# Performance work log

Measured on AMD Instinct MI355X. Metric: run time of the kernel, lower is better.

Reference implementation:

```python
import jax, jax.numpy as jnp
import numpy as np

NGRAM = 16
SUB = 512  # bytes per sub-block


def byte2image(block, ngram=NGRAM):
    """block: (B, L) int -> (B, 1, ngram*8, L-ngram) float32 in [-1, 1]."""
    B, L = block.shape
    blk = block.astype(jnp.int32)
    # nxt[:, i] = blk[:, i+1], last column zero
    nxt = jnp.concatenate([blk[:, 1:], jnp.zeros((B, 1), jnp.int32)], axis=1)
    # 8 bit-shifted views of the byte stream
    shifts = jnp.stack(
        [((blk << s) & 255) + ((nxt >> (8 - s)) & 255) for s in range(8)],
        axis=1,
    )  # (B, 8, L)
    flat = shifts.reshape(B, -1)  # (B, 8*L)
    parts = [flat] + [jnp.roll(flat, -i, axis=1) for i in range(1, ngram)]
    stacked = jnp.concatenate(parts, axis=1).reshape(B, ngram * 8, L)
    result = stacked[:, :, :-ngram].astype(jnp.float32)
    result = (result / 255.0 - 0.5) / 0.5
    return result[:, None]  # (B, 1, ngram*8, L-ngram)


def byte2image_4k(block, ngram=NGRAM):
    """block: (B, 4096) -> (B, 8, ngram*8, 512-ngram)."""
    return jnp.concatenate(
        [byte2image(block[:, i * SUB:(i + 1) * SUB], ngram) for i in range(8)],
        axis=1,
    )


def setup_inputs() -> dict:
    key = jax.random.key(0)
    kx, kw = jax.random.split(key)
    x = jax.random.randint(kx, (256, 4096), 0, 256, dtype=jnp.int64)
    W = jax.random.normal(kw, (496, 64), dtype=jnp.float32) * 0.02
    return {"x": x, "W": W}


def reference(x, W):
    # ByteFormerWrapper.forward with block_size=4096: byte2image_4k then the
    # (opaque) model; model stood in by a linear head over the image width.
    img = byte2image_4k(x)                      # (B, 8, 128, 496)
    out = jnp.einsum('bchw,wo->bcho', img, W)   # (B, 8, 128, 64)
    return out
```

## Files before the change

kernel.cpp:

```cpp
#include <hip/hip_runtime.h>

typedef unsigned short u16;
typedef unsigned int u32;
typedef _Float16 half8 __attribute__((ext_vector_type(8)));
typedef __attribute__((ext_vector_type(4))) float floatx4;

#define LSTRIDE 72
#define BIMG (128 * LSTRIDE)

__global__ __launch_bounds__(256, 2) void byteformer_fused(
    const int* __restrict__ x, const float* __restrict__ Wm,
    float* __restrict__ out) {
  __shared__ __align__(16) u16 arena[4 * BIMG];
  __shared__ float part[256];
  __shared__ float csumsh[64];

  const int t = threadIdx.x;
  const int mtile = blockIdx.x;
  const int y = blockIdx.y;

  const int wave = t >> 6, lane = t & 63;
  const int wm = wave >> 1, wn = wave & 1;
  const int quad = lane >> 4, l16 = lane & 15;

  const int sA_sub = t >> 4;
  const int sA_kg  = (t >> 1) & 7;
  const int sA_qh  = t & 1;
  const long xrow = ((long)mtile * 16 + sA_sub) * 512;

  floatx4 acc[4][4];
  #pragma unroll
  for (int mt = 0; mt < 4; ++mt)
    #pragma unroll
    for (int nt = 0; nt < 4; ++nt)
      acc[mt][nt] = floatx4{0.f, 0.f, 0.f, 0.f};

  float csum_local = 0.0f;

  int4 ca, cb; int cc;
  float f[17];

  auto xload = [&](int kc) {
    const int base = kc * 64 + sA_kg * 8;
    ca = *(const int4*)&x[xrow + base];
    cb = *(const int4*)&x[xrow + base + 4];
    cc = (base + 8 < 512) ? x[xrow + base + 8] : 0;
  };

  auto wload = [&](int kc) {
    const int cbase = kc * 64 + 16 * wave - 2 * y - 1;
    #pragma unroll
    for (int j = 0; j < 17; ++j) {
      const int c = cbase + j;
      f[j] = (c >= 0 && c < 496) ? Wm[c * 64 + lane] : 0.0f;
    }
  };

  auto astage = [&](u16* dstb) {
    const u32 c0 = (u32)ca.x, c1 = (u32)ca.y, c2 = (u32)ca.z, c3 = (u32)ca.w;
    const u32 c4 = (u32)cb.x, c5 = (u32)cb.y, c6 = (u32)cb.z, c7 = (u32)cb.w;
    const u32 c8 = (u32)cc;
    const u32 P0 = ((c0 << 8) | c1) | (((c1 << 8) | c2) << 16);
    const u32 P1 = ((c2 << 8) | c3) | (((c3 << 8) | c4) << 16);
    const u32 P2 = ((c4 << 8) | c5) | (((c5 << 8) | c6) << 16);
    const u32 P3 = ((c6 << 8) | c7) | (((c7 << 8) | c8) << 16);
    u16* arow = &dstb[(sA_sub * 8 + sA_qh * 4) * LSTRIDE + sA_kg * 8];
    #pragma unroll
    for (int qi = 0; qi < 4; ++qi) {
      const int sh = 8 - (sA_qh * 4 + qi);
      int4 d;
      d.x = (int)(((P0 >> sh) & 0x00FF00FFu) | 0x64006400u);
      d.y = (int)(((P1 >> sh) & 0x00FF00FFu) | 0x64006400u);
      d.z = (int)(((P2 >> sh) & 0x00FF00FFu) | 0x64006400u);
      d.w = (int)(((P3 >> sh) & 0x00FF00FFu) | 0x64006400u);
      *(int4*)(arow + qi * LSTRIDE) = d;
    }
  };

  auto bstage = [&](u16* dstb) {
    u16 h[17];
    #pragma unroll
    for (int j = 0; j < 17; ++j)
      h[j] = __builtin_bit_cast(unsigned short, (_Float16)f[j]);
    #pragma unroll
    for (int j = 1; j <= 16; ++j) csum_local += f[j];
    #pragma unroll
    for (int g = 0; g < 2; ++g) {
      const int mgrp = 2 * wave + g;
      #pragma unroll
      for (int pp = 0; pp < 2; ++pp) {
        const int jb = g * 8 + 1 - pp;
        int4 d;
        d.x = (int)((u32)h[jb + 0] | ((u32)h[jb + 1] << 16));
        d.y = (int)((u32)h[jb + 2] | ((u32)h[jb + 3] << 16));
        d.z = (int)((u32)h[jb + 4] | ((u32)h[jb + 5] << 16));
        d.w = (int)((u32)h[jb + 6] | ((u32)h[jb + 7] << 16));
        *(int4*)&dstb[(pp * 64 + lane) * LSTRIDE + mgrp * 8] = d;
      }
    }
  };

  auto compute = [&](const u16* Ab, const u16* Bb) {
    #pragma unroll
    for (int ks = 0; ks < 2; ++ks) {
      const int koff = ks * 32 + quad * 8;
      half8 af[4], bf[4];
      #pragma unroll
      for (int mt = 0; mt < 4; ++mt)
        af[mt] = *(const half8*)&Ab[(wm * 64 + mt * 16 + l16) * LSTRIDE + koff];
      #pragma unroll
      for (int nt = 0; nt < 4; ++nt)
        bf[nt] = *(const half8*)&Bb[(wn * 64 + nt * 16 + l16) * LSTRIDE + koff];
      #pragma unroll
      for (int mt = 0; mt < 4; ++mt)
        #pragma unroll
        for (int nt = 0; nt < 4; ++nt)
          acc[mt][nt] = __builtin_amdgcn_mfma_f32_16x16x32_f16(
              af[mt], bf[nt], acc[mt][nt], 0, 0, 0);
    }
  };

  xload(0); wload(0);
  astage(arena); bstage(arena + 2 * BIMG);
  __syncthreads();

  #pragma unroll
  for (int kc = 0; kc < 8; ++kc) {
    u16* Acur = arena + (kc & 1) * BIMG;
    u16* Bcur = arena + (2 + (kc & 1)) * BIMG;
    u16* Anxt = arena + ((kc + 1) & 1) * BIMG;
    u16* Bnxt = arena + (2 + ((kc + 1) & 1)) * BIMG;
    if (kc < 7) { xload(kc + 1); wload(kc + 1); }
    compute(Acur, Bcur);
    if (kc < 7) { astage(Anxt); bstage(Bnxt); }
    __syncthreads();
  }

  const float S = 2.0f / 255.0f;
  const float K1 = 1024.0f * S + 1.0f;
  part[t] = csum_local;
  __syncthreads();
  if (t < 64)
    csumsh[t] = K1 * (part[t] + part[t + 64] + part[t + 128] + part[t + 192]);
  __syncthreads();

  float cs[4];
  #pragma unroll
  for (int nt = 0; nt < 4; ++nt) cs[nt] = csumsh[nt * 16 + l16];

  float* ep = (float*)arena;
  #pragma unroll
  for (int mt = 0; mt < 4; ++mt) {
    #pragma unroll
    for (int i = 0; i < 4; ++i) {
      const int mr = wm * 64 + mt * 16 + quad * 4 + i;
      const int sub_l = mr >> 3, q = mr & 7;
      const int rowbase = sub_l * 1040 + wn * 512 + q * 64 + l16;
      #pragma unroll
      for (int nt = 0; nt < 4; ++nt)
        ep[rowbase + nt * 16] = S * acc[mt][nt][i] - cs[nt];
    }
  }
  __syncthreads();

  const long outbase = (long)mtile * 16 * 8192 + (long)y * 1024;
  #pragma unroll
  for (int k2 = 0; k2 < 16; ++k2) {
    const float4 v =
        *(const float4*)((const char*)ep + k2 * 4160 + wave * 1024 + lane * 16);
    *(float4*)&out[outbase + (long)k2 * 8192 + wave * 256 + lane * 4] = v;
  }
}

extern "C" void kernel_launch(void* const* d_in, const int* in_sizes, int n_in,
                              void* d_out, int out_size, void* d_ws, size_t ws_size,
                              hipStream_t stream) {
  const int* x = (const int*)d_in[0];
  const float* Wm = (const float*)d_in[1];
  float* out = (float*)d_out;
  byteformer_fused<<<dim3(128, 8), dim3(256), 0, stream>>>(x, Wm, out);
}
```

Measured before the change: 108.7 us.

## Single-buffer LDS tiles, split W loads across k-steps, raise occupancy to 4 blocks

Shared memory drops from a double-buffered A/B arena to one A and one B tile, and launch bounds rise from 2 to 4 blocks per CU to get more waves resident. W loads are split into two halves whose latency is hidden behind the two MFMA k-steps, and the fp16 packing is done early into packed registers. The epilogue runs in two halves so it fits in the smaller arena. The cost is an extra barrier per k-chunk with no LDS double buffering, and tighter register limits that could cause spills.

```diff
diff --git a/kernel.cpp b/kernel.cpp
--- a/kernel.cpp
+++ b/kernel.cpp
@@ -6,14 +6,16 @@
 typedef __attribute__((ext_vector_type(4))) float floatx4;
 
 #define LSTRIDE 72
-#define BIMG (128 * LSTRIDE)
-
-__global__ __launch_bounds__(256, 2) void byteformer_fused(
+#define TILE (128 * LSTRIDE)
+
+__global__ __launch_bounds__(256, 4) void byteformer_fused(
     const int* __restrict__ x, const float* __restrict__ Wm,
     float* __restrict__ out) {
-  __shared__ __align__(16) u16 arena[4 * BIMG];
+  __shared__ __align__(16) u16 arena[2 * TILE];
   __shared__ float part[256];
   __shared__ float csumsh[64];
+  u16* As = arena;
+  u16* Bs = arena + TILE;
 
   const int t = threadIdx.x;
   const int mtile = blockIdx.x;
@@ -38,7 +40,8 @@
   float csum_local = 0.0f;
 
   int4 ca, cb; int cc;
-  float f[17];
+  float fv[17];
+  u32 hp[9];
 
   auto xload = [&](int kc) {
     const int base = kc * 64 + sA_kg * 8;
@@ -47,16 +50,45 @@
     cc = (base + 8 < 512) ? x[xrow + base + 8] : 0;
   };
 
-  auto wload = [&](int kc) {
+  auto wissueA = [&](int kc) {
     const int cbase = kc * 64 + 16 * wave - 2 * y - 1;
     #pragma unroll
-    for (int j = 0; j < 17; ++j) {
+    for (int j = 0; j < 9; ++j) {
       const int c = cbase + j;
-      f[j] = (c >= 0 && c < 496) ? Wm[c * 64 + lane] : 0.0f;
-    }
-  };
-
-  auto astage = [&](u16* dstb) {
+      fv[j] = (c >= 0 && c < 496) ? Wm[c * 64 + lane] : 0.0f;
+    }
+  };
+  auto wissueB = [&](int kc) {
+    const int cbase = kc * 64 + 16 * wave - 2 * y - 1;
+    #pragma unroll
+    for (int j = 9; j < 17; ++j) {
+      const int c = cbase + j;
+      fv[j] = (c >= 0 && c < 496) ? Wm[c * 64 + lane] : 0.0f;
+    }
+  };
+  auto wfinishA = [&]() {
+    #pragma unroll
+    for (int j = 1; j <= 8; ++j) csum_local += fv[j];
+    #pragma unroll
+    for (int i = 0; i < 4; ++i) {
+      u32 h0 = __builtin_bit_cast(unsigned short, (_Float16)fv[2 * i]);
+      u32 h1 = __builtin_bit_cast(unsigned short, (_Float16)fv[2 * i + 1]);
+      hp[i] = h0 | (h1 << 16);
+    }
+  };
+  auto wfinishB = [&]() {
+    #pragma unroll
+    for (int j = 9; j <= 16; ++j) csum_local += fv[j];
+    #pragma unroll
+    for (int i = 4; i < 8; ++i) {
+      u32 h0 = __builtin_bit_cast(unsigned short, (_Float16)fv[2 * i]);
+      u32 h1 = __builtin_bit_cast(unsigned short, (_Float16)fv[2 * i + 1]);
+      hp[i] = h0 | (h1 << 16);
+    }
+    hp[8] = (u32)__builtin_bit_cast(unsigned short, (_Float16)fv[16]);
+  };
+
+  auto astage = [&]() {
     const u32 c0 = (u32)ca.x, c1 = (u32)ca.y, c2 = (u32)ca.z, c3 = (u32)ca.w;
     const u32 c4 = (u32)cb.x, c5 = (u32)cb.y, c6 = (u32)cb.z, c7 = (u32)cb.w;
     const u32 c8 = (u32)cc;
@@ -64,7 +96,7 @@
     const u32 P1 = ((c2 << 8) | c3) | (((c3 << 8) | c4) << 16);
     const u32 P2 = ((c4 << 8) | c5) | (((c5 << 8) | c6) << 16);
     const u32 P3 = ((c6 << 8) | c7) | (((c7 << 8) | c8) << 16);
-    u16* arow = &dstb[(sA_sub * 8 + sA_qh * 4) * LSTRIDE + sA_kg * 8];
+    u16* arow = &As[(sA_sub * 8 + sA_qh * 4) * LSTRIDE + sA_kg * 8];
     #pragma unroll
     for (int qi = 0; qi < 4; ++qi) {
       const int sh = 8 - (sA_qh * 4 + qi);
@@ -77,63 +109,55 @@
     }
   };
 
-  auto bstage = [&](u16* dstb) {
-    u16 h[17];
-    #pragma unroll
-    for (int j = 0; j < 17; ++j)
-      h[j] = __builtin_bit_cast(unsigned short, (_Float16)f[j]);
-    #pragma unroll
-    for (int j = 1; j <= 16; ++j) csum_local += f[j];
+  auto bstage = [&]() {
     #pragma unroll
     for (int g = 0; g < 2; ++g) {
       const int mgrp = 2 * wave + g;
-      #pragma unroll
-      for (int pp = 0; pp < 2; ++pp) {
-        const int jb = g * 8 + 1 - pp;
-        int4 d;
-        d.x = (int)((u32)h[jb + 0] | ((u32)h[jb + 1] << 16));
-        d.y = (int)((u32)h[jb + 2] | ((u32)h[jb + 3] << 16));
-        d.z = (int)((u32)h[jb + 4] | ((u32)h[jb + 5] << 16));
-        d.w = (int)((u32)h[jb + 6] | ((u32)h[jb + 7] << 16));
-        *(int4*)&dstb[(pp * 64 + lane) * LSTRIDE + mgrp * 8] = d;
-      }
-    }
-  };
-
-  auto compute = [&](const u16* Ab, const u16* Bb) {
-    #pragma unroll
-    for (int ks = 0; ks < 2; ++ks) {
-      const int koff = ks * 32 + quad * 8;
-      half8 af[4], bf[4];
-      #pragma unroll
-      for (int mt = 0; mt < 4; ++mt)
-        af[mt] = *(const half8*)&Ab[(wm * 64 + mt * 16 + l16) * LSTRIDE + koff];
+      int4 d1;
+      d1.x = (int)hp[4 * g + 0];
+      d1.y = (int)hp[4 * g + 1];
+      d1.z = (int)hp[4 * g + 2];
+      d1.w = (int)hp[4 * g + 3];
+      *(int4*)&Bs[(64 + lane) * LSTRIDE + mgrp * 8] = d1;
+      int4 d0;
+      d0.x = (int)((hp[4 * g + 0] >> 16) | (hp[4 * g + 1] << 16));
+      d0.y = (int)((hp[4 * g + 1] >> 16) | (hp[4 * g + 2] << 16));
+      d0.z = (int)((hp[4 * g + 2] >> 16) | (hp[4 * g + 3] << 16));
+      d0.w = (int)((hp[4 * g + 3] >> 16) | (hp[4 * g + 4] << 16));
+      *(int4*)&Bs[lane * LSTRIDE + mgrp * 8] = d0;
+    }
+  };
+
+  auto compute_ks = [&](int ks) {
+    const int koff = ks * 32 + quad * 8;
+    half8 bf[4];
+    #pragma unroll
+    for (int nt = 0; nt < 4; ++nt)
+      bf[nt] = *(const half8*)&Bs[(wn * 64 + nt * 16 + l16) * LSTRIDE + koff];
+    #pragma unroll
+    for (int mt = 0; mt < 4; ++mt) {
+      half8 af = *(const half8*)&As[(wm * 64 + mt * 16 + l16) * LSTRIDE + koff];
       #pragma unroll
       for (int nt = 0; nt < 4; ++nt)
-        bf[nt] = *(const half8*)&Bb[(wn * 64 + nt * 16 + l16) * LSTRIDE + koff];
-      #pragma unroll
-      for (int mt = 0; mt < 4; ++mt)
-        #pragma unroll
-        for (int nt = 0; nt < 4; ++nt)
-          acc[mt][nt] = __builtin_amdgcn_mfma_f32_16x16x32_f16(
-              af[mt], bf[nt], acc[mt][nt], 0, 0, 0);
-    }
-  };
-
-  xload(0); wload(0);
-  astage(arena); bstage(arena + 2 * BIMG);
-  __syncthreads();
-
-  #pragma unroll
+        acc[mt][nt] = __builtin_amdgcn_mfma_f32_16x16x32_f16(
+            af, bf[nt], acc[mt][nt], 0, 0, 0);
+    }
+  };
+
+  xload(0);
+  wissueA(0); wissueB(0);
+  wfinishA(); wfinishB();
+
   for (int kc = 0; kc < 8; ++kc) {
-    u16* Acur = arena + (kc & 1) * BIMG;
-    u16* Bcur = arena + (2 + (kc & 1)) * BIMG;
-    u16* Anxt = arena + ((kc + 1) & 1) * BIMG;
-    u16* Bnxt = arena + (2 + ((kc + 1) & 1)) * BIMG;
-    if (kc < 7) { xload(kc + 1); wload(kc + 1); }
-    compute(Acur, Bcur);
-    if (kc < 7) { astage(Anxt); bstage(Bnxt); }
     __syncthreads();
+    astage();
+    bstage();
+    __syncthreads();
+    if (kc < 7) { xload(kc + 1); wissueA(kc + 1); }
+    compute_ks(0);
+    if (kc < 7) { wfinishA(); wissueB(kc + 1); }
+    compute_ks(1);
+    if (kc < 7) { wfinishB(); }
   }
 
   const float S = 2.0f / 255.0f;
@@ -150,25 +174,29 @@
 
   float* ep = (float*)arena;
   #pragma unroll
-  for (int mt = 0; mt < 4; ++mt) {
-    #pragma unroll
-    for (int i = 0; i < 4; ++i) {
-      const int mr = wm * 64 + mt * 16 + quad * 4 + i;
-      const int sub_l = mr >> 3, q = mr & 7;
-      const int rowbase = sub_l * 1040 + wn * 512 + q * 64 + l16;
+  for (int h = 0; h < 2; ++h) {
+    if (wm == h) {
       #pragma unroll
-      for (int nt = 0; nt < 4; ++nt)
-        ep[rowbase + nt * 16] = S * acc[mt][nt][i] - cs[nt];
-    }
-  }
-  __syncthreads();
-
-  const long outbase = (long)mtile * 16 * 8192 + (long)y * 1024;
-  #pragma unroll
-  for (int k2 = 0; k2 < 16; ++k2) {
-    const float4 v =
-        *(const float4*)((const char*)ep + k2 * 4160 + wave * 1024 + lane * 16);
-    *(float4*)&out[outbase + (long)k2 * 8192 + wave * 256 + lane * 4] = v;
+      for (int mt = 0; mt < 4; ++mt)
+        #pragma unroll
+        for (int i = 0; i < 4; ++i) {
+          const int mr = mt * 16 + quad * 4 + i;
+          const int rowbase = (mr >> 3) * 1040 + wn * 512 + (mr & 7) * 64 + l16;
+          #pragma unroll
+          for (int nt = 0; nt < 4; ++nt)
+            ep[rowbase + nt * 16] = __builtin_fmaf(S, acc[mt][nt][i], -cs[nt]);
+        }
+    }
+    __syncthreads();
+    const long outb =
+        ((long)mtile * 16 + (long)h * 8) * 8192 + (long)y * 1024;
+    #pragma unroll
+    for (int k2 = 0; k2 < 8; ++k2) {
+      const float4 v =
+          *(const float4*)((const char*)ep + k2 * 4160 + wave * 1024 + lane * 16);
+      *(float4*)&out[outb + (long)k2 * 8192 + wave * 256 + lane * 4] = v;
+    }
+    if (h == 0) __syncthreads();
   }
 }
 
```

Measured after the change: 118.1 us. +8.6%, slower.
